# Performance work log

Hardware: AMD Instinct MI355X
Metric: run time of the kernel (lower is better)

## Reference

```python
import jax, jax.numpy as jnp
import numpy as np
import math

D_MODEL = 512
N_HEADS = 8
D_FF = 2048
TOP_FACTOR = 5
LN_EPS = 1e-5


def _layernorm(x, g, b):
    m = jnp.mean(x, axis=-1, keepdims=True)
    v = jnp.mean((x - m) ** 2, axis=-1, keepdims=True)
    return (x - m) / jnp.sqrt(v + LN_EPS) * g + b


def _prob_sparse_attn(q_in, k_in, v_in, wq, bq, wk, bk, wv, bv, wo, bo):
    # weights stored (in, out): y = x @ w + b  (equivalent to torch Linear)
    B, Lq, dm = q_in.shape
    Lk = k_in.shape[1]
    H, D = N_HEADS, dm // N_HEADS
    q = (q_in @ wq + bq).reshape(B, Lq, H, D).transpose(0, 2, 1, 3)  # (B,H,Lq,D)
    k = (k_in @ wk + bk).reshape(B, Lk, H, D).transpose(0, 2, 1, 3)
    v = (v_in @ wv + bv).reshape(B, Lk, H, D).transpose(0, 2, 1, 3)

    qn = q / jnp.linalg.norm(q, axis=-1, keepdims=True)
    kn = k / jnp.linalg.norm(k, axis=-1, keepdims=True)
    # full cosine-similarity matrix, reduced to a row mean (as in the original)
    scores_all = jnp.einsum('bhqd,bhkd->bhqk', qn, kn)
    mean_scores = scores_all.mean(axis=-1)  # (B,H,Lq)

    u = max(1, Lq // TOP_FACTOR)
    _, top_idx = jax.lax.top_k(mean_scores, u)  # (B,H,u)

    q_sel = jnp.take_along_axis(q, top_idx[..., None], axis=2)  # (B,H,u,D)
    scores = jnp.einsum('bhud,bhkd->bhuk', q_sel, k) / math.sqrt(D)
    attn = jax.nn.softmax(scores, axis=-1)
    ctx_sel = jnp.einsum('bhuk,bhkd->bhud', attn, v)  # (B,H,u,D)

    b_ix = jnp.arange(B)[:, None, None]
    h_ix = jnp.arange(H)[None, :, None]
    context = jnp.zeros((B, H, Lq, D), dtype=q.dtype).at[b_ix, h_ix, top_idx].set(ctx_sel)
    out = context.transpose(0, 2, 1, 3).reshape(B, Lq, dm)
    return out @ wo + bo


def _decoder_layer(x, enc_out, p):
    xn = _layernorm(x, p['ln1_g'], p['ln1_b'])
    x = x + _prob_sparse_attn(xn, xn, xn, p['sa_wq'], p['sa_bq'], p['sa_wk'], p['sa_bk'],
                              p['sa_wv'], p['sa_bv'], p['sa_wo'], p['sa_bo'])
    xn = _layernorm(x, p['ln2_g'], p['ln2_b'])
    x = x + _prob_sparse_attn(xn, enc_out, enc_out, p['ca_wq'], p['ca_bq'], p['ca_wk'], p['ca_bk'],
                              p['ca_wv'], p['ca_bv'], p['ca_wo'], p['ca_bo'])
    xn = _layernorm(x, p['ln3_g'], p['ln3_b'])
    h = jax.nn.relu(xn @ p['ff_w1'] + p['ff_b1'])
    return x + (h @ p['ff_w2'] + p['ff_b2'])


def setup_inputs() -> dict:
    key = jax.random.key(0)
    ks = iter(jax.random.split(key, 32))
    B, L = 2, 2048
    dm, dff = D_MODEL, D_FF
    s = 1.0 / math.sqrt(dm)
    inp = {
        'x': jax.random.normal(next(ks), (B, L, dm), jnp.float32),
        'enc_out': jax.random.normal(next(ks), (B, L, dm), jnp.float32),
    }
    for pre in ('sa', 'ca'):
        for nm in ('wq', 'wk', 'wv', 'wo'):
            inp[f'{pre}_{nm}'] = jax.random.normal(next(ks), (dm, dm), jnp.float32) * s
            inp[f'{pre}_{nm[1:] and "b" + nm[1:]}'] = jnp.zeros((dm,), jnp.float32)
    inp['ff_w1'] = jax.random.normal(next(ks), (dm, dff), jnp.float32) * s
    inp['ff_b1'] = jnp.zeros((dff,), jnp.float32)
    inp['ff_w2'] = jax.random.normal(next(ks), (dff, dm), jnp.float32) / math.sqrt(dff)
    inp['ff_b2'] = jnp.zeros((dm,), jnp.float32)
    for i in (1, 2, 3):
        inp[f'ln{i}_g'] = jnp.ones((dm,), jnp.float32)
        inp[f'ln{i}_b'] = jnp.zeros((dm,), jnp.float32)
    return inp


def reference(x, enc_out,
              sa_wq, sa_bq, sa_wk, sa_bk, sa_wv, sa_bv, sa_wo, sa_bo,
              ca_wq, ca_bq, ca_wk, ca_bk, ca_wv, ca_bv, ca_wo, ca_bo,
              ff_w1, ff_b1, ff_w2, ff_b2,
              ln1_g, ln1_b, ln2_g, ln2_b, ln3_g, ln3_b):
    p = dict(sa_wq=sa_wq, sa_bq=sa_bq, sa_wk=sa_wk, sa_bk=sa_bk, sa_wv=sa_wv, sa_bv=sa_bv,
             sa_wo=sa_wo, sa_bo=sa_bo, ca_wq=ca_wq, ca_bq=ca_bq, ca_wk=ca_wk, ca_bk=ca_bk,
             ca_wv=ca_wv, ca_bv=ca_bv, ca_wo=ca_wo, ca_bo=ca_bo,
             ff_w1=ff_w1, ff_b1=ff_b1, ff_w2=ff_w2, ff_b2=ff_b2,
             ln1_g=ln1_g, ln1_b=ln1_b, ln2_g=ln2_g, ln2_b=ln2_b, ln3_g=ln3_g, ln3_b=ln3_b)
    return _decoder_layer(x, enc_out, p)
```

## Files before the change

### kernel.cpp

```cpp
#include <hip/hip_runtime.h>

#define BB 2
#define LL 2048
#define DM 512
#define NH 8
#define DH 64
#define DFF 2048
#define UU 409
#define ROWS (BB*LL)
#define X_ELEMS 2097152
#define NCHUNK 16

typedef unsigned short u16;
typedef __attribute__((ext_vector_type(8))) short short8;
typedef __attribute__((ext_vector_type(4))) float floatx4;

#define G_TOTAL 38200000
__device__ float g_buf[G_TOTAL];
__device__ int   g_isbf16;

#define A_Q     10495488
#define A_K     12592640
#define A_V     14689792
#define A_MKN   25175552
#define A_MS    25176576
#define A_SEL   25209344
#define A_PARTK 25242112
#define A_LIST  25274880
#define A_PO    25281536
#define A_PML   33670144
#define A_CTXF  16786944
#define XN_H    16796672
#define XN_L    18893824
#define CTX_H   33573888
#define CTX_L   35671040
#define ENC_H   37768192
#define ENC_L   39865344
#define AH_H    41962496
#define WT_SAQKV 67864576
#define WT_SAO   69437440
#define WT_CAQ   69961728
#define WT_CAK   70486016
#define WT_CAV   71010304
#define WT_CAO   71534592
#define WT_W1    72058880
#define WT_W2    74156032

__constant__ int c_end[28] = {
    2097152, 4194304, 4456448, 4456960, 4719104, 4719616, 4981760, 4982272,
    5244416, 5244928, 5507072, 5507584, 5769728, 5770240, 6032384, 6032896,
    6295040, 6295552, 7344128, 7346176, 8394752, 8395264, 8395776, 8396288,
    8396800, 8397312, 8397824, 8398336
};
__constant__ int sm_idx[16] = {3,5,7,9,11,13,15,17,19,21,22,23,24,25,26,27};
__constant__ int sm_cum[16] = {64,128,192,256,320,384,448,512,768,832,896,960,1024,1088,1152,1216};
#define XG 262144
#define EG 262144
#define SG 1216

__device__ __forceinline__ float bf2f(u16 x) {
    union { unsigned int u; float f; } c; c.u = ((unsigned int)x) << 16; return c.f;
}
__device__ __forceinline__ u16 f2bf(float f) {
    union { float f; unsigned int u; } c; c.f = f;
    unsigned int u = c.u;
    return (u16)((u + 0x7FFFu + ((u >> 16) & 1u)) >> 16);
}

struct P28 { const void* p[28]; };
struct I3 { int v[3]; };

__global__ void cvt_all(P28 ps) {
    const int f = (((const u16*)ps.p[22])[0] == 0x3F80u) ? 1 : 0;
    if (blockIdx.x == 0 && threadIdx.x == 0) g_isbf16 = f;
    u16* gb16 = (u16*)g_buf;
    int stride = gridDim.x * blockDim.x;
    for (int g = blockIdx.x * blockDim.x + threadIdx.x; g < XG + EG + SG; g += stride) {
        if (g < XG) {
            int e = g * 8;
            if (f) {
                uint4 raw = ((const uint4*)ps.p[0])[g];
                const u16* rr = (const u16*)&raw;
                float v[8] __attribute__((aligned(16)));
#pragma unroll
                for (int i = 0; i < 8; i++) v[i] = bf2f(rr[i]);
                *(float4*)(g_buf + e) = ((const float4*)v)[0];
                *(float4*)(g_buf + e + 4) = ((const float4*)v)[1];
            } else {
                *(uint4*)(g_buf + e)     = ((const uint4*)ps.p[0])[g * 2];
                *(uint4*)(g_buf + e + 4) = ((const uint4*)ps.p[0])[g * 2 + 1];
            }
        } else if (g < XG + EG) {
            int gl = g - XG;
            int e = gl * 8;
            float v[8] __attribute__((aligned(16)));
            if (f) {
                uint4 raw = ((const uint4*)ps.p[1])[gl];
                const u16* rr = (const u16*)&raw;
#pragma unroll
                for (int i = 0; i < 8; i++) v[i] = bf2f(rr[i]);
            } else {
                *(float4*)(v)     = ((const float4*)ps.p[1])[gl * 2];
                *(float4*)(v + 4) = ((const float4*)ps.p[1])[gl * 2 + 1];
            }
            u16 hh[8] __attribute__((aligned(16)));
            u16 lo[8] __attribute__((aligned(16)));
#pragma unroll
            for (int i = 0; i < 8; i++) { u16 hi = f2bf(v[i]); hh[i] = hi; lo[i] = f2bf(v[i] - bf2f(hi)); }
            *(uint4*)(&gb16[ENC_H + e]) = *(const uint4*)hh;
            *(uint4*)(&gb16[ENC_L + e]) = *(const uint4*)lo;
        } else {
            int t = g - XG - EG;
            int si = 0;
            while (t >= sm_cum[si]) si++;
            int s = sm_idx[si];
            int gl = t - (si ? sm_cum[si - 1] : 0);
            int e = gl * 8;
            float* dst = g_buf + c_end[s - 1] + e;
            if (f) {
                uint4 raw = *(const uint4*)((const u16*)ps.p[s] + e);
                const u16* rr = (const u16*)&raw;
#pragma unroll
                for (int i = 0; i < 8; i++) dst[i] = bf2f(rr[i]);
            } else {
                *(uint4*)(dst)     = *(const uint4*)((const float*)ps.p[s] + e);
                *(uint4*)(dst + 4) = *(const uint4*)((const float*)ps.p[s] + e + 4);
            }
        }
    }
}

__constant__ int tj[10][6] = {
    {2,  WT_SAQKV, 0,    512,  786432, 8},
    {4,  WT_SAQKV, 512,  512,  786432, 8},
    {6,  WT_SAQKV, 1024, 512,  786432, 8},
    {8,  WT_SAO,   0,    512,  262144, 8},
    {10, WT_CAQ,   0,    512,  262144, 8},
    {12, WT_CAK,   0,    512,  262144, 8},
    {14, WT_CAV,   0,    512,  262144, 8},
    {16, WT_CAO,   0,    512,  262144, 8},
    {18, WT_W1,    0,    512, 1048576, 32},
    {20, WT_W2,    0,   2048, 1048576, 8},
};
__constant__ int tcum[10] = {64, 128, 192, 256, 320, 384, 448, 512, 768, 1024};
__global__ void transpose_all(P28 ps) {
    const int f = (((const u16*)ps.p[22])[0] == 0x3F80u) ? 1 : 0;
    int bid = blockIdx.x;
    int j = 0;
    while (bid >= tcum[j]) j++;
    int t = bid - (j ? tcum[j - 1] : 0);
    int widx = tj[j][0], wt = tj[j][1], col0 = tj[j][2];
    int K = tj[j][3], lo = tj[j][4], txn = tj[j][5];
    int Nsrc = txn * 64;
    int n0 = (t % txn) * 64, k0 = (t / txn) * 64;
    __shared__ float tb[64][65];
    int c = threadIdx.x & 63, r0 = threadIdx.x >> 6;
    const void* W = ps.p[widx];
    u16* WTh = ((u16*)g_buf) + wt;
    for (int i = 0; i < 16; i++) {
        int r = r0 + 4 * i;
        size_t src = (size_t)(k0 + r) * Nsrc + n0 + c;
        tb[r][c] = f ? bf2f(((const u16*)W)[src]) : ((const float*)W)[src];
    }
    __syncthreads();
    for (int i = 0; i < 16; i++) {
        int r = r0 + 4 * i;
        float v = tb[c][r];
        u16 hi = f2bf(v);
        size_t o = (size_t)(col0 + n0 + r) * K + k0 + c;
        WTh[o] = hi;
        WTh[lo + o] = f2bf(v - bf2f(hi));
    }
}

__global__ void lnorm_k(int x_off, int g_off, int b_off, int yh_u16, int yl_u16) {
    int row = blockIdx.x;
    int tid = threadIdx.x;
    const float* x = g_buf + x_off + (size_t)row * DM;
    float a = x[tid], c = x[tid + 256];
    float s1 = a + c, s2 = a * a + c * c;
    for (int o = 32; o > 0; o >>= 1) { s1 += __shfl_xor(s1, o); s2 += __shfl_xor(s2, o); }
    __shared__ float r1[4], r2[4];
    int wave = tid >> 6, lane = tid & 63;
    if (lane == 0) { r1[wave] = s1; r2[wave] = s2; }
    __syncthreads();
    s1 = r1[0] + r1[1] + r1[2] + r1[3];
    s2 = r2[0] + r2[1] + r2[2] + r2[3];
    float mean = s1 * (1.0f / DM);
    float var  = s2 * (1.0f / DM) - mean * mean;
    float rstd = rsqrtf(var + 1e-5f);
    const float* gg = g_buf + g_off;
    const float* bb = g_buf + b_off;
    u16* yh = ((u16*)g_buf) + yh_u16 + (size_t)row * DM;
    u16* yl = ((u16*)g_buf) + yl_u16 + (size_t)row * DM;
    float v1 = (a - mean) * rstd * gg[tid]       + bb[tid];
    float v2 = (c - mean) * rstd * gg[tid + 256] + bb[tid + 256];
    u16 h1 = f2bf(v1), h2 = f2bf(v2);
    yh[tid] = h1;       yl[tid] = f2bf(v1 - bf2f(h1));
    yh[tid + 256] = h2; yl[tid + 256] = f2bf(v2 - bf2f(h2));
}

template<int WM, bool SPLIT, bool ALZ, bool SEC, bool RELU, bool RESID, bool FINAL, bool OUTH>
__global__ void mgemm_k(int a_u16, int wt_u16_off, I3 boffs, int resid_off,
                        int out_off, void* __restrict__ dext, int M, int N, int K) {
    constexpr int BT_M = WM * 32;
    constexpr int A4 = BT_M * 4;
    __shared__ u16 Ash[BT_M * 40];
    __shared__ u16 Asl[SPLIT ? BT_M * 40 : 8];
    __shared__ u16 Bsh[128 * 40];
    __shared__ u16 Bsl[SPLIT ? 128 * 40 : 8];
    const u16* Ah = ((const u16*)g_buf) + a_u16;
    const u16* Al = Ah + (size_t)M * K;
    const u16* WTh = ((const u16*)g_buf) + wt_u16_off;
    const u16* WTl = WTh + (size_t)N * K;
    const int isbf = g_isbf16;
    const bool use_bl = SPLIT && !isbf;
    const bool use_al = SPLIT && !(ALZ && isbf);
    int tid = threadIdx.x;
    int lane = tid & 63, wid = tid >> 6;
    int wm = wid >> 1, wn = wid & 1;
    int quad = lane >> 4, l15 = lane & 15;
    int m0 = blockIdx.y * BT_M, n0 = blockIdx.x * 128;
    floatx4 acc[WM][4];
#pragma unroll
    for (int i = 0; i < WM; i++)
#pragma unroll
        for (int j = 0; j < 4; j++) acc[i][j] = (floatx4){0.f, 0.f, 0.f, 0.f};
    for (int k0 = 0; k0 < K; k0 += 32) {
#pragma unroll
        for (int i = 0; i < (A4 + 255) / 256; i++) {
            int idx8 = tid + 256 * i;
            if (A4 % 256 == 0 || idx8 < A4) {
                int r = idx8 >> 2, c8 = (idx8 & 3) * 8;
                *(uint4*)(&Ash[r * 40 + c8]) = *(const uint4*)(Ah + (size_t)(m0 + r) * K + k0 + c8);
                if (SPLIT && use_al)
                    *(uint4*)(&Asl[r * 40 + c8]) = *(const uint4*)(Al + (size_t)(m0 + r) * K + k0 + c8);
            }
        }
#pragma unroll
        for (int i = 0; i < 2; i++) {
            int idx8 = tid + 256 * i;
            int r = idx8 >> 2, c8 = (idx8 & 3) * 8;
            *(uint4*)(&Bsh[r * 40 + c8]) = *(const uint4*)(WTh + (size_t)(n0 + r) * K + k0 + c8);
            if (SPLIT && use_bl)
                *(uint4*)(&Bsl[r * 40 + c8]) = *(const uint4*)(WTl + (size_t)(n0 + r) * K + k0 + c8);
        }
        __syncthreads();
        short8 ah[WM], bh[4], al[WM], bl[4];
#pragma unroll
        for (int i = 0; i < WM; i++) {
            int ro = (wm * WM * 16 + i * 16 + l15) * 40 + quad * 8;
            ah[i] = *(const short8*)(&Ash[ro]);
            if (SPLIT && use_al) al[i] = *(const short8*)(&Asl[ro]);
        }
#pragma unroll
        for (int j = 0; j < 4; j++) {
            int ro = (wn * 64 + j * 16 + l15) * 40 + quad * 8;
            bh[j] = *(const short8*)(&Bsh[ro]);
            if (SPLIT && use_bl) bl[j] = *(const short8*)(&Bsl[ro]);
        }
#pragma unroll
        for (int i = 0; i < WM; i++)
#pragma unroll
            for (int j = 0; j < 4; j++) {
                acc[i][j] = __builtin_amdgcn_mfma_f32_16x16x32_bf16(ah[i], bh[j], acc[i][j], 0, 0, 0);
                if constexpr (SPLIT) {
                    if (use_bl)
                        acc[i][j] = __builtin_amdgcn_mfma_f32_16x16x32_bf16(ah[i], bl[j], acc[i][j], 0, 0, 0);
                    if (use_al)
                        acc[i][j] = __builtin_amdgcn_mfma_f32_16x16x32_bf16(al[i], bh[j], acc[i][j], 0, 0, 0);
                }
            }
        __syncthreads();
    }
#pragma unroll
    for (int i = 0; i < WM; i++)
#pragma unroll
        for (int j = 0; j < 4; j++)
#pragma unroll
            for (int r = 0; r < 4; r++) {
                int row = m0 + wm * WM * 16 + i * 16 + quad * 4 + r;
                int col = n0 + wn * 64 + j * 16 + l15;
                int sec = SEC ? (col >> 9) : 0;
                int ci  = SEC ? (col & 511) : col;
                float v = acc[i][j][r] + g_buf[boffs.v[sec] + ci];
                if (RELU) v = fmaxf(v, 0.f);
                if (RESID) v += g_buf[resid_off + (size_t)row * N + col];
                if (FINAL) {
                    if (isbf) ((u16*)dext)[(size_t)row * N + col] = f2bf(v);
                    else      ((float*)dext)[(size_t)row * N + col] = v;
                } else if (OUTH) {
                    ((u16*)g_buf)[out_off + (size_t)row * N + col] = f2bf(v);
                } else if (SEC) {
                    g_buf[out_off + ((size_t)sec * ROWS + row) * 512 + ci] = v;
                } else {
                    g_buf[out_off + (size_t)row * N + col] = v;
                }
            }
}

__global__ void meankn_p1(int k_off, int part_off) {
    int bh = blockIdx.x >> 5, chunk = blockIdx.x & 31;
    int b = bh >> 3, h = bh & 7;
    int wave = threadIdx.x >> 6, lane = threadIdx.x & 63;
    const float* base = g_buf + k_off + (size_t)b * LL * DM + (size_t)h * DH + lane;
    float acc = 0.f;
    for (int t = 0; t < 16; t++) {
        int j = chunk * 64 + wave * 16 + t;
        float kv = base[(size_t)j * DM];
        float s = kv * kv;
        for (int o = 32; o > 0; o >>= 1) s += __shfl_xor(s, o);
        acc += kv / sqrtf(fmaxf(s, 1e-30f));
    }
    __shared__ float red[4][64];
    red[wave][lane] = acc;
    __syncthreads();
    if (threadIdx.x < 64)
        g_buf[part_off + (size_t)blockIdx.x * 64 + threadIdx.x] =
            red[0][threadIdx.x] + red[1][threadIdx.x] + red[2][threadIdx.x] + red[3][threadIdx.x];
}
__global__ void meankn_p2(int part_off, int mkn_off) {
    int bh = blockIdx.x; int lane = threadIdx.x;
    float s = 0.f;
    for (int c = 0; c < 32; c++) s += g_buf[part_off + (size_t)(bh * 32 + c) * 64 + lane];
    g_buf[mkn_off + bh * 64 + lane] = s * (1.0f / LL);
}

__global__ void mscore_k(int q_off, int mkn_off, int ms_off) {
    int row = blockIdx.x * 4 + (threadIdx.x >> 6);
    int lane = threadIdx.x & 63;
    int q = row & (LL - 1);
    int bh = row >> 11;
    int b = bh >> 3, h = bh & 7;
    float qv = g_buf[q_off + ((size_t)b * LL + q) * DM + h * DH + lane];
    float m = g_buf[mkn_off + bh * 64 + lane];
    float s = qv * qv, d = qv * m;
    for (int o = 32; o > 0; o >>= 1) { s += __shfl_xor(s, o); d += __shfl_xor(d, o); }
    if (lane == 0) g_buf[ms_off + row] = d / sqrtf(fmaxf(s, 1e-30f));
}

__global__ void topsel_k(int ms_off, int sel_off, int u) {
    __shared__ float s[LL];
    int bh = blockIdx.y, chunk = blockIdx.x;
    for (int i = threadIdx.x; i < LL; i += 256) s[i] = g_buf[ms_off + bh * LL + i];
    __syncthreads();
    int il = threadIdx.x >> 2;
    int i = chunk * 64 + il;
    int jq = threadIdx.x & 3;
    float si = s[i];
    int cnt = 0;
    for (int t = 0; t < 512; t++) {
        int j = jq * 512 + t;
        float sj = s[j];
        cnt += (sj > si) || (sj == si && j < i);
    }
    cnt += __shfl_xor(cnt, 1);
    cnt += __shfl_xor(cnt, 2);
    if (jq == 0) ((int*)(g_buf + sel_off))[bh * LL + i] = (cnt < u) ? 1 : 0;
}

__global__ void compact_k(int sel_off, int list_off) {
    __shared__ int cnts[256];
    __shared__ int pref[256];
    int bh = blockIdx.x, tid = threadIdx.x;
    const int* sel = (const int*)(g_buf + sel_off) + bh * LL;
    int* list = (int*)(g_buf + list_off) + bh * 416;
    int c = 0;
    for (int j = 0; j < 8; j++) c += sel[tid * 8 + j];
    cnts[tid] = c;
    __syncthreads();
    if (tid == 0) { int run = 0; for (int i = 0; i < 256; i++) { pref[i] = run; run += cnts[i]; } }
    __syncthreads();
    int base = pref[tid];
    for (int j = 0; j < 8; j++) {
        int i = tid * 8 + j;
        if (sel[i]) list[base++] = i;
    }
}

__global__ void zero_k(int off, int n) {
    int i = blockIdx.x * blockDim.x + threadIdx.x;
    int st = gridDim.x * blockDim.x;
    for (; i < n; i += st) g_buf[off + i] = 0.f;
}

__global__ __launch_bounds__(256, 2) void attn_flash(int q_off, int k_off, int v_off,
        int list_off, int po_off, int pml_off, int u) {
    int bh = blockIdx.y, b = bh >> 3, h = bh & 7;
    int chunk = blockIdx.z;
    int tid = threadIdx.x, lane = tid & 63, w = tid >> 6;
    int quad = lane >> 4, l15 = lane & 15;
    const int* list = (const int*)(g_buf + list_off);

    short8 qh[4][2], ql[4][2];
#pragma unroll
    for (int g = 0; g < 4; g++) {
        int slot_q = blockIdx.x * 256 + w * 64 + g * 16 + l15;
        int qidx = list[bh * 416 + (slot_q < u ? slot_q : u - 1)];
        const float* qp = g_buf + q_off + ((size_t)b * LL + qidx) * DM + h * DH;
#pragma unroll
        for (int d2 = 0; d2 < 2; d2++) {
            float v[8] __attribute__((aligned(16)));
            *(float4*)(v)     = *(const float4*)(qp + d2 * 32 + quad * 8);
            *(float4*)(v + 4) = *(const float4*)(qp + d2 * 32 + quad * 8 + 4);
            u16 hh[8] __attribute__((aligned(16)));
            u16 lo[8] __attribute__((aligned(16)));
#pragma unroll
            for (int j = 0; j < 8; j++) {
                float s = v[j] * 0.125f;
                u16 hi = f2bf(s); hh[j] = hi; lo[j] = f2bf(s - bf2f(hi));
            }
            qh[g][d2] = *(const short8*)hh; ql[g][d2] = *(const short8*)lo;
        }
    }

    __shared__ u16 Ksh[64 * 68], Ksl[64 * 68];
    __shared__ u16 Vth[64 * 68], Vtl[64 * 68];
    __shared__ float smbuf[4352];

    float m_run[4][4], l_run[4][4];
    floatx4 acc_o[4][4];
#pragma unroll
    for (int g = 0; g < 4; g++)
#pragma unroll
        for (int r = 0; r < 4; r++) {
            m_run[g][r] = -3.0e38f; l_run[g][r] = 0.f;
            acc_o[g][r] = (floatx4){0.f, 0.f, 0.f, 0.f};
        }

    for (int kt = 0; kt < 2; kt++) {
        int row0 = chunk * 128 + kt * 64;
        __syncthreads();
        {
            int tok = tid >> 2, c = (tid & 3) * 16;
            const float* kp = g_buf + k_off + ((size_t)(b * LL + row0 + tok)) * DM + h * DH + c;
            float v[16] __attribute__((aligned(16)));
#pragma unroll
            for (int i = 0; i < 4; i++) *(float4*)(v + 4 * i) = *(const float4*)(kp + 4 * i);
            u16 hh[16] __attribute__((aligned(16)));
            u16 lo[16] __attribute__((aligned(16)));
#pragma unroll
            for (int i = 0; i < 16; i++) { u16 hi = f2bf(v[i]); hh[i] = hi; lo[i] = f2bf(v[i] - bf2f(hi)); }
            *(uint4*)(&Ksh[tok * 68 + c])     = ((const uint4*)hh)[0];
            *(uint4*)(&Ksh[tok * 68 + c + 8]) = ((const uint4*)hh)[1];
            *(uint4*)(&Ksl[tok * 68 + c])     = ((const uint4*)lo)[0];
            *(uint4*)(&Ksl[tok * 68 + c + 8]) = ((const uint4*)lo)[1];
            const float* vp = g_buf + v_off + ((size_t)(b * LL + row0 + tok)) * DM + h * DH + c;
#pragma unroll
            for (int i = 0; i < 4; i++)
                *(float4*)(&smbuf[tok * 68 + c + 4 * i]) = *(const float4*)(vp + 4 * i);
        }
        __syncthreads();
        {
            int d = tid >> 2, ck = (tid & 3) * 16;
            u16 hh[16] __attribute__((aligned(16)));
            u16 lo[16] __attribute__((aligned(16)));
#pragma unroll
            for (int i = 0; i < 16; i++) {
                float x = smbuf[(ck + i) * 68 + d];
                u16 hi = f2bf(x); hh[i] = hi; lo[i] = f2bf(x - bf2f(hi));
            }
            *(uint4*)(&Vth[d * 68 + ck])     = ((const uint4*)hh)[0];
            *(uint4*)(&Vth[d * 68 + ck + 8]) = ((const uint4*)hh)[1];
            *(uint4*)(&Vtl[d * 68 + ck])     = ((const uint4*)lo)[0];
            *(uint4*)(&Vtl[d * 68 + ck + 8]) = ((const uint4*)lo)[1];
        }
        __syncthreads();
        float* ps = smbuf + w * 1088;
#pragma unroll
        for (int g = 0; g < 4; g++) {
            floatx4 sacc[4];
#pragma unroll
            for (int t = 0; t < 4; t++) {
                sacc[t] = (floatx4){0.f, 0.f, 0.f, 0.f};
#pragma unroll
                for (int d2 = 0; d2 < 2; d2++) {
                    int ro = (t * 16 + l15) * 68 + d2 * 32 + quad * 8;
                    short8 kh = *(const short8*)(&Ksh[ro]);
                    short8 kl = *(const short8*)(&Ksl[ro]);
                    sacc[t] = __builtin_amdgcn_mfma_f32_16x16x32_bf16(qh[g][d2], kh, sacc[t], 0, 0, 0);
                    sacc[t] = __builtin_amdgcn_mfma_f32_16x16x32_bf16(qh[g][d2], kl, sacc[t], 0, 0, 0);
                    sacc[t] = __builtin_amdgcn_mfma_f32_16x16x32_bf16(ql[g][d2], kh, sacc[t], 0, 0, 0);
                }
            }
            float alpha[4];
#pragma unroll
            for (int r = 0; r < 4; r++) {
                float mx = fmaxf(fmaxf(sacc[0][r], sacc[1][r]), fmaxf(sacc[2][r], sacc[3][r]));
                for (int o = 1; o < 16; o <<= 1) mx = fmaxf(mx, __shfl_xor(mx, o));
                float mn = fmaxf(m_run[g][r], mx);
                alpha[r] = __expf(m_run[g][r] - mn);
                m_run[g][r] = mn;
                float ls = 0.f;
#pragma unroll
                for (int t = 0; t < 4; t++) {
                    float p = __expf(sacc[t][r] - mn);
                    sacc[t][r] = p;
                    ls += p;
                }
                for (int o = 1; o < 16; o <<= 1) ls += __shfl_xor(ls, o);
                l_run[g][r] = l_run[g][r] * alpha[r] + ls;
            }
#pragma unroll
            for (int t = 0; t < 4; t++)
#pragma unroll
                for (int r = 0; r < 4; r++)
                    ps[(quad * 4 + r) * 68 + t * 16 + l15] = sacc[t][r];
#pragma unroll
            for (int j = 0; j < 4; j++)
#pragma unroll
                for (int r = 0; r < 4; r++) acc_o[g][j][r] *= alpha[r];
#pragma unroll
            for (int s2 = 0; s2 < 2; s2++) {
                float pv[8] __attribute__((aligned(16)));
                *(float4*)(pv)     = *(const float4*)(&ps[l15 * 68 + s2 * 32 + quad * 8]);
                *(float4*)(pv + 4) = *(const float4*)(&ps[l15 * 68 + s2 * 32 + quad * 8 + 4]);
                u16 ph[8] __attribute__((aligned(16)));
                u16 pl[8] __attribute__((aligned(16)));
#pragma unroll
                for (int j = 0; j < 8; j++) { u16 hi = f2bf(pv[j]); ph[j] = hi; pl[j] = f2bf(pv[j] - bf2f(hi)); }
                short8 phv = *(const short8*)ph, plv = *(const short8*)pl;
#pragma unroll
                for (int j = 0; j < 4; j++) {
                    int ro = (j * 16 + l15) * 68 + s2 * 32 + quad * 8;
                    short8 vh = *(const short8*)(&Vth[ro]);
                    short8 vl = *(const short8*)(&Vtl[ro]);
                    acc_o[g][j] = __builtin_amdgcn_mfma_f32_16x16x32_bf16(phv, vh, acc_o[g][j], 0, 0, 0);
                    acc_o[g][j] = __builtin_amdgcn_mfma_f32_16x16x32_bf16(phv, vl, acc_o[g][j], 0, 0, 0);
                    acc_o[g][j] = __builtin_amdgcn_mfma_f32_16x16x32_bf16(plv, vh, acc_o[g][j], 0, 0, 0);
                }
            }
        }
    }
#pragma unroll
    for (int g = 0; g < 4; g++)
#pragma unroll
        for (int r = 0; r < 4; r++) {
            int slot = blockIdx.x * 256 + w * 64 + g * 16 + quad * 4 + r;
            if (slot >= u) continue;
            size_t rec = ((size_t)(bh * 16 + chunk)) * 512 + slot;
            float* po = g_buf + po_off + rec * 64;
#pragma unroll
            for (int j = 0; j < 4; j++) po[j * 16 + l15] = acc_o[g][j][r];
            if (l15 == 0) {
                float* pml = g_buf + pml_off + rec * 2;
                pml[0] = m_run[g][r]; pml[1] = l_run[g][r];
            }
        }
}

__global__ void attn_combine(int po_off, int pml_off, int list_off, int u) {
    int bh = blockIdx.y;
    int b = bh >> 3, h = bh & 7;
    int tid = threadIdx.x;
    int qi = tid >> 4;
    int kb = tid & 15;
    int ds = kb * 4;
    int slot = blockIdx.x * 16 + qi;
    if (slot >= u) return;
    int qidx = ((const int*)(g_buf + list_off))[bh * 416 + slot];
    float m = -3.0e38f;
#pragma unroll
    for (int c = 0; c < NCHUNK; c++)
        m = fmaxf(m, g_buf[pml_off + (((size_t)(bh * 16 + c)) * 512 + slot) * 2]);
    float l = 0.f, O0 = 0.f, O1 = 0.f, O2 = 0.f, O3 = 0.f;
#pragma unroll
    for (int c = 0; c < NCHUNK; c++) {
        size_t rec = ((size_t)(bh * 16 + c)) * 512 + slot;
        const float* pml = g_buf + pml_off + rec * 2;
        float a = __expf(pml[0] - m);
        l += a * pml[1];
        float4 o = *(const float4*)(g_buf + po_off + rec * 64 + ds);
        O0 += a * o.x; O1 += a * o.y; O2 += a * o.z; O3 += a * o.w;
    }
    float inv = 1.0f / l;
    float o0 = O0 * inv, o1 = O1 * inv, o2 = O2 * inv, o3 = O3 * inv;
    size_t idx = ((size_t)b * LL + qidx) * DM + h * DH + ds;
    ushort4 hv, lv;
    hv.x = f2bf(o0); lv.x = f2bf(o0 - bf2f(hv.x));
    hv.y = f2bf(o1); lv.y = f2bf(o1 - bf2f(hv.y));
    hv.z = f2bf(o2); lv.z = f2bf(o2 - bf2f(hv.z));
    hv.w = f2bf(o3); lv.w = f2bf(o3 - bf2f(hv.w));
    *(ushort4*)(((u16*)g_buf) + CTX_H + idx) = hv;
    *(ushort4*)(((u16*)g_buf) + CTX_L + idx) = lv;
}

extern "C" void kernel_launch(void* const* d_in, const int* in_sizes, int n_in,
                              void* d_out, int out_size, void* d_ws, size_t ws_size,
                              hipStream_t stream) {
    static const int SZ[28] = {
        2097152, 2097152,
        262144, 512, 262144, 512, 262144, 512, 262144, 512,
        262144, 512, 262144, 512, 262144, 512, 262144, 512,
        1048576, 2048, 1048576, 512,
        512, 512, 512, 512, 512, 512
    };
    int OFF[28];
    int cur = 0;
    for (int i = 0; i < 28; i++) { OFF[i] = cur; cur += SZ[i]; }

    P28 ps;
    for (int i = 0; i < 28; i++) ps.p[i] = d_in[i];
    cvt_all<<<2048, 256, 0, stream>>>(ps);
    transpose_all<<<1024, 256, 0, stream>>>(ps);

    auto select_attend = [&](void) {
        meankn_p1<<<16 * 32, 256, 0, stream>>>(A_K, A_PARTK);
        meankn_p2<<<16, 64, 0, stream>>>(A_PARTK, A_MKN);
        mscore_k<<<(BB * NH * LL) / 4, 256, 0, stream>>>(A_Q, A_MKN, A_MS);
        topsel_k<<<dim3(32, 16), 256, 0, stream>>>(A_MS, A_SEL, UU);
        compact_k<<<BB * NH, 256, 0, stream>>>(A_SEL, A_LIST);
        zero_k<<<1024, 256, 0, stream>>>(A_CTXF, X_ELEMS);
        attn_flash<<<dim3(2, 16, NCHUNK), 256, 0, stream>>>(A_Q, A_K, A_V, A_LIST, A_PO, A_PML, UU);
        attn_combine<<<dim3(26, 16), 256, 0, stream>>>(A_PO, A_PML, A_LIST, UU);
    };

    lnorm_k<<<ROWS, 256, 0, stream>>>(OFF[0], OFF[22], OFF[23], XN_H, XN_L);
    mgemm_k<2, true, false, true, false, false, false, false><<<dim3(12, 64), 256, 0, stream>>>(
        XN_H, WT_SAQKV, I3{{OFF[3], OFF[5], OFF[7]}}, 0, A_Q, nullptr, ROWS, 1536, 512);
    select_attend();
    mgemm_k<1, true, false, false, false, true, false, false><<<dim3(4, 128), 256, 0, stream>>>(
        CTX_H, WT_SAO, I3{{OFF[9], 0, 0}}, OFF[0], OFF[0], nullptr, ROWS, 512, 512);

    lnorm_k<<<ROWS, 256, 0, stream>>>(OFF[0], OFF[24], OFF[25], XN_H, XN_L);
    mgemm_k<1, true, false, false, false, false, false, false><<<dim3(4, 128), 256, 0, stream>>>(
        XN_H, WT_CAQ, I3{{OFF[11], 0, 0}}, 0, A_Q, nullptr, ROWS, 512, 512);
    mgemm_k<1, true, true, false, false, false, false, false><<<dim3(4, 128), 256, 0, stream>>>(
        ENC_H, WT_CAK, I3{{OFF[13], 0, 0}}, 0, A_K, nullptr, ROWS, 512, 512);
    mgemm_k<1, false, false, false, false, false, false, false><<<dim3(4, 128), 256, 0, stream>>>(
        ENC_H, WT_CAV, I3{{OFF[15], 0, 0}}, 0, A_V, nullptr, ROWS, 512, 512);
    select_attend();
    mgemm_k<1, false, false, false, false, true, false, false><<<dim3(4, 128), 256, 0, stream>>>(
        CTX_H, WT_CAO, I3{{OFF[17], 0, 0}}, OFF[0], OFF[0], nullptr, ROWS, 512, 512);

    lnorm_k<<<ROWS, 256, 0, stream>>>(OFF[0], OFF[26], OFF[27], XN_H, XN_L);
    mgemm_k<4, false, false, false, true, false, false, true><<<dim3(16, 32), 256, 0, stream>>>(
        XN_H, WT_W1, I3{{OFF[19], 0, 0}}, 0, AH_H, nullptr, ROWS, 2048, 512);
    mgemm_k<1, false, false, false, false, true, true, false><<<dim3(4, 128), 256, 0, stream>>>(
        AH_H, WT_W2, I3{{OFF[21], 0, 0}}, OFF[0], 0, d_out, ROWS, 512, 2048);
}
```

Before: 585.3 us.

## Fuse prep kernels, merge cross-attn K/V GEMM, and cut sparse-attention launches

Merges the input conversion and weight transpose into one prep kernel, and fuses the cross-attention K and V projections into a single sectioned GEMM. It folds mean-key reduction into the score kernel and has top-k selection write the compact list and rank directly, dropping the compact and zero kernels. The combine step zero-fills unselected rows itself. Attention blocks are made smaller (more blocks), and cross-attention drops the third bf16 split product. The aim is fewer launches and less redundant work, at the cost of some precision in cross-attention and more indexing logic.

```diff
diff --git a/kernel.cpp b/kernel.cpp
--- a/kernel.cpp
+++ b/kernel.cpp
@@ -24,7 +24,7 @@
 #define A_V     14689792
 #define A_MKN   25175552
 #define A_MS    25176576
-#define A_SEL   25209344
+#define A_RANK  25209344
 #define A_PARTK 25242112
 #define A_LIST  25274880
 #define A_PO    25281536
@@ -40,8 +40,7 @@
 #define WT_SAQKV 67864576
 #define WT_SAO   69437440
 #define WT_CAQ   69961728
-#define WT_CAK   70486016
-#define WT_CAV   71010304
+#define WT_CAKV  70486016
 #define WT_CAO   71534592
 #define WT_W1    72058880
 #define WT_W2    74156032
@@ -70,12 +69,54 @@
 struct P28 { const void* p[28]; };
 struct I3 { int v[3]; };
 
-__global__ void cvt_all(P28 ps) {
+__constant__ int tj[10][6] = {
+    {2,  WT_SAQKV, 0,    512,  786432, 8},
+    {4,  WT_SAQKV, 512,  512,  786432, 8},
+    {6,  WT_SAQKV, 1024, 512,  786432, 8},
+    {8,  WT_SAO,   0,    512,  262144, 8},
+    {10, WT_CAQ,   0,    512,  262144, 8},
+    {12, WT_CAKV,  0,    512,  524288, 8},
+    {14, WT_CAKV,  512,  512,  524288, 8},
+    {16, WT_CAO,   0,    512,  262144, 8},
+    {18, WT_W1,    0,    512, 1048576, 32},
+    {20, WT_W2,    0,   2048, 1048576, 8},
+};
+__constant__ int tcum[10] = {64, 128, 192, 256, 320, 384, 448, 512, 768, 1024};
+__global__ void prep_all(P28 ps) {
     const int f = (((const u16*)ps.p[22])[0] == 0x3F80u) ? 1 : 0;
     if (blockIdx.x == 0 && threadIdx.x == 0) g_isbf16 = f;
     u16* gb16 = (u16*)g_buf;
-    int stride = gridDim.x * blockDim.x;
-    for (int g = blockIdx.x * blockDim.x + threadIdx.x; g < XG + EG + SG; g += stride) {
+    if (blockIdx.x < 1024) {
+        int bid = blockIdx.x;
+        int j = 0;
+        while (bid >= tcum[j]) j++;
+        int t = bid - (j ? tcum[j - 1] : 0);
+        int widx = tj[j][0], wt = tj[j][1], col0 = tj[j][2];
+        int K = tj[j][3], lo = tj[j][4], txn = tj[j][5];
+        int Nsrc = txn * 64;
+        int n0 = (t % txn) * 64, k0 = (t / txn) * 64;
+        __shared__ float tb[64][65];
+        int c = threadIdx.x & 63, r0 = threadIdx.x >> 6;
+        const void* W = ps.p[widx];
+        u16* WTh = gb16 + wt;
+        for (int i = 0; i < 16; i++) {
+            int r = r0 + 4 * i;
+            size_t src = (size_t)(k0 + r) * Nsrc + n0 + c;
+            tb[r][c] = f ? bf2f(((const u16*)W)[src]) : ((const float*)W)[src];
+        }
+        __syncthreads();
+        for (int i = 0; i < 16; i++) {
+            int r = r0 + 4 * i;
+            float v = tb[c][r];
+            u16 hi = f2bf(v);
+            size_t o = (size_t)(col0 + n0 + r) * K + k0 + c;
+            WTh[o] = hi;
+            WTh[lo + o] = f2bf(v - bf2f(hi));
+        }
+        return;
+    }
+    int stride = 2048 * blockDim.x;
+    for (int g = (blockIdx.x - 1024) * blockDim.x + threadIdx.x; g < XG + EG + SG; g += stride) {
         if (g < XG) {
             int e = g * 8;
             if (f) {
@@ -127,49 +168,6 @@
                 *(uint4*)(dst + 4) = *(const uint4*)((const float*)ps.p[s] + e + 4);
             }
         }
-    }
-}
-
-__constant__ int tj[10][6] = {
-    {2,  WT_SAQKV, 0,    512,  786432, 8},
-    {4,  WT_SAQKV, 512,  512,  786432, 8},
-    {6,  WT_SAQKV, 1024, 512,  786432, 8},
-    {8,  WT_SAO,   0,    512,  262144, 8},
-    {10, WT_CAQ,   0,    512,  262144, 8},
-    {12, WT_CAK,   0,    512,  262144, 8},
-    {14, WT_CAV,   0,    512,  262144, 8},
-    {16, WT_CAO,   0,    512,  262144, 8},
-    {18, WT_W1,    0,    512, 1048576, 32},
-    {20, WT_W2,    0,   2048, 1048576, 8},
-};
-__constant__ int tcum[10] = {64, 128, 192, 256, 320, 384, 448, 512, 768, 1024};
-__global__ void transpose_all(P28 ps) {
-    const int f = (((const u16*)ps.p[22])[0] == 0x3F80u) ? 1 : 0;
-    int bid = blockIdx.x;
-    int j = 0;
-    while (bid >= tcum[j]) j++;
-    int t = bid - (j ? tcum[j - 1] : 0);
-    int widx = tj[j][0], wt = tj[j][1], col0 = tj[j][2];
-    int K = tj[j][3], lo = tj[j][4], txn = tj[j][5];
-    int Nsrc = txn * 64;
-    int n0 = (t % txn) * 64, k0 = (t / txn) * 64;
-    __shared__ float tb[64][65];
-    int c = threadIdx.x & 63, r0 = threadIdx.x >> 6;
-    const void* W = ps.p[widx];
-    u16* WTh = ((u16*)g_buf) + wt;
-    for (int i = 0; i < 16; i++) {
-        int r = r0 + 4 * i;
-        size_t src = (size_t)(k0 + r) * Nsrc + n0 + c;
-        tb[r][c] = f ? bf2f(((const u16*)W)[src]) : ((const float*)W)[src];
-    }
-    __syncthreads();
-    for (int i = 0; i < 16; i++) {
-        int r = r0 + 4 * i;
-        float v = tb[c][r];
-        u16 hi = f2bf(v);
-        size_t o = (size_t)(col0 + n0 + r) * K + k0 + c;
-        WTh[o] = hi;
-        WTh[lo + o] = f2bf(v - bf2f(hi));
     }
 }
 
@@ -200,8 +198,8 @@
     yh[tid + 256] = h2; yl[tid + 256] = f2bf(v2 - bf2f(h2));
 }
 
-template<int WM, bool SPLIT, bool ALZ, bool SEC, bool RELU, bool RESID, bool FINAL, bool OUTH>
-__global__ void mgemm_k(int a_u16, int wt_u16_off, I3 boffs, int resid_off,
+template<int WM, bool SPLIT, bool SEC, bool RELU, bool RESID, bool FINAL, bool OUTH>
+__global__ void mgemm_k(I3 a_offs, I3 splt, I3 alz, int wt_u16_off, I3 boffs, int resid_off,
                         int out_off, void* __restrict__ dext, int M, int N, int K) {
     constexpr int BT_M = WM * 32;
     constexpr int A4 = BT_M * 4;
@@ -209,13 +207,14 @@
     __shared__ u16 Asl[SPLIT ? BT_M * 40 : 8];
     __shared__ u16 Bsh[128 * 40];
     __shared__ u16 Bsl[SPLIT ? 128 * 40 : 8];
-    const u16* Ah = ((const u16*)g_buf) + a_u16;
+    int sec_blk = SEC ? ((blockIdx.x * 128) >> 9) : 0;
+    const u16* Ah = ((const u16*)g_buf) + a_offs.v[sec_blk];
     const u16* Al = Ah + (size_t)M * K;
     const u16* WTh = ((const u16*)g_buf) + wt_u16_off;
     const u16* WTl = WTh + (size_t)N * K;
     const int isbf = g_isbf16;
-    const bool use_bl = SPLIT && !isbf;
-    const bool use_al = SPLIT && !(ALZ && isbf);
+    const bool use_al = SPLIT && splt.v[sec_blk] && !(alz.v[sec_blk] && isbf);
+    const bool use_bl = SPLIT && splt.v[sec_blk] && !isbf;
     int tid = threadIdx.x;
     int lane = tid & 63, wid = tid >> 6;
     int wm = wid >> 1, wn = wid & 1;
@@ -287,8 +286,8 @@
                 if (RELU) v = fmaxf(v, 0.f);
                 if (RESID) v += g_buf[resid_off + (size_t)row * N + col];
                 if (FINAL) {
-                    if (isbf) ((u16*)dext)[(size_t)row * N + col] = f2bf(v);
-                    else      ((float*)dext)[(size_t)row * N + col] = v;
+                    if (g_isbf16) ((u16*)dext)[(size_t)row * N + col] = f2bf(v);
+                    else          ((float*)dext)[(size_t)row * N + col] = v;
                 } else if (OUTH) {
                     ((u16*)g_buf)[out_off + (size_t)row * N + col] = f2bf(v);
                 } else if (SEC) {
@@ -319,27 +318,30 @@
         g_buf[part_off + (size_t)blockIdx.x * 64 + threadIdx.x] =
             red[0][threadIdx.x] + red[1][threadIdx.x] + red[2][threadIdx.x] + red[3][threadIdx.x];
 }
-__global__ void meankn_p2(int part_off, int mkn_off) {
-    int bh = blockIdx.x; int lane = threadIdx.x;
-    float s = 0.f;
-    for (int c = 0; c < 32; c++) s += g_buf[part_off + (size_t)(bh * 32 + c) * 64 + lane];
-    g_buf[mkn_off + bh * 64 + lane] = s * (1.0f / LL);
-}
-
-__global__ void mscore_k(int q_off, int mkn_off, int ms_off) {
-    int row = blockIdx.x * 4 + (threadIdx.x >> 6);
-    int lane = threadIdx.x & 63;
-    int q = row & (LL - 1);
-    int bh = row >> 11;
-    int b = bh >> 3, h = bh & 7;
-    float qv = g_buf[q_off + ((size_t)b * LL + q) * DM + h * DH + lane];
-    float m = g_buf[mkn_off + bh * 64 + lane];
-    float s = qv * qv, d = qv * m;
-    for (int o = 32; o > 0; o >>= 1) { s += __shfl_xor(s, o); d += __shfl_xor(d, o); }
-    if (lane == 0) g_buf[ms_off + row] = d / sqrtf(fmaxf(s, 1e-30f));
-}
-
-__global__ void topsel_k(int ms_off, int sel_off, int u) {
+
+__global__ void mscore_k(int q_off, int part_off, int ms_off) {
+    int bh = blockIdx.y, b = bh >> 3, h = bh & 7;
+    int tid = threadIdx.x;
+    __shared__ float mk[64];
+    if (tid < 64) {
+        float s = 0.f;
+        for (int c = 0; c < 32; c++) s += g_buf[part_off + (size_t)(bh * 32 + c) * 64 + tid];
+        mk[tid] = s * (1.0f / LL);
+    }
+    __syncthreads();
+    int w = tid >> 6, lane = tid & 63;
+    float m = mk[lane];
+#pragma unroll
+    for (int it = 0; it < 8; it++) {
+        int row = blockIdx.x * 32 + it * 4 + w;
+        float qv = g_buf[q_off + ((size_t)b * LL + row) * DM + h * DH + lane];
+        float s = qv * qv, d = qv * m;
+        for (int o = 32; o > 0; o >>= 1) { s += __shfl_xor(s, o); d += __shfl_xor(d, o); }
+        if (lane == 0) g_buf[ms_off + bh * LL + row] = d / sqrtf(fmaxf(s, 1e-30f));
+    }
+}
+
+__global__ void topsel_k(int ms_off, int list_off, int rank_off, int u) {
     __shared__ float s[LL];
     int bh = blockIdx.y, chunk = blockIdx.x;
     for (int i = threadIdx.x; i < LL; i += 256) s[i] = g_buf[ms_off + bh * LL + i];
@@ -356,35 +358,16 @@
     }
     cnt += __shfl_xor(cnt, 1);
     cnt += __shfl_xor(cnt, 2);
-    if (jq == 0) ((int*)(g_buf + sel_off))[bh * LL + i] = (cnt < u) ? 1 : 0;
-}
-
-__global__ void compact_k(int sel_off, int list_off) {
-    __shared__ int cnts[256];
-    __shared__ int pref[256];
-    int bh = blockIdx.x, tid = threadIdx.x;
-    const int* sel = (const int*)(g_buf + sel_off) + bh * LL;
-    int* list = (int*)(g_buf + list_off) + bh * 416;
-    int c = 0;
-    for (int j = 0; j < 8; j++) c += sel[tid * 8 + j];
-    cnts[tid] = c;
-    __syncthreads();
-    if (tid == 0) { int run = 0; for (int i = 0; i < 256; i++) { pref[i] = run; run += cnts[i]; } }
-    __syncthreads();
-    int base = pref[tid];
-    for (int j = 0; j < 8; j++) {
-        int i = tid * 8 + j;
-        if (sel[i]) list[base++] = i;
-    }
-}
-
-__global__ void zero_k(int off, int n) {
-    int i = blockIdx.x * blockDim.x + threadIdx.x;
-    int st = gridDim.x * blockDim.x;
-    for (; i < n; i += st) g_buf[off + i] = 0.f;
-}
-
-__global__ __launch_bounds__(256, 2) void attn_flash(int q_off, int k_off, int v_off,
+    if (jq == 0) {
+        int* list = (int*)(g_buf + list_off);
+        int* rank = (int*)(g_buf + rank_off);
+        if (cnt < u) { list[bh * 416 + cnt] = i; rank[bh * LL + i] = cnt; }
+        else rank[bh * LL + i] = -1;
+    }
+}
+
+template<bool S3>
+__global__ __launch_bounds__(256) void attn_flash(int q_off, int k_off, int v_off,
         int list_off, int po_off, int pml_off, int u) {
     int bh = blockIdx.y, b = bh >> 3, h = bh & 7;
     int chunk = blockIdx.z;
@@ -392,10 +375,10 @@
     int quad = lane >> 4, l15 = lane & 15;
     const int* list = (const int*)(g_buf + list_off);
 
-    short8 qh[4][2], ql[4][2];
-#pragma unroll
-    for (int g = 0; g < 4; g++) {
-        int slot_q = blockIdx.x * 256 + w * 64 + g * 16 + l15;
+    short8 qh[2][2], ql[2][2];
+#pragma unroll
+    for (int g = 0; g < 2; g++) {
+        int slot_q = blockIdx.x * 128 + w * 32 + g * 16 + l15;
         int qidx = list[bh * 416 + (slot_q < u ? slot_q : u - 1)];
         const float* qp = g_buf + q_off + ((size_t)b * LL + qidx) * DM + h * DH;
 #pragma unroll
@@ -414,14 +397,16 @@
         }
     }
 
-    __shared__ u16 Ksh[64 * 68], Ksl[64 * 68];
-    __shared__ u16 Vth[64 * 68], Vtl[64 * 68];
+    __shared__ u16 Ksh[64 * 68];
+    __shared__ u16 Ksl[S3 ? 64 * 68 : 8];
+    __shared__ u16 Vth[64 * 68];
+    __shared__ u16 Vtl[S3 ? 64 * 68 : 8];
     __shared__ float smbuf[4352];
 
-    float m_run[4][4], l_run[4][4];
-    floatx4 acc_o[4][4];
-#pragma unroll
-    for (int g = 0; g < 4; g++)
+    float m_run[2][4], l_run[2][4];
+    floatx4 acc_o[2][4];
+#pragma unroll
+    for (int g = 0; g < 2; g++)
 #pragma unroll
         for (int r = 0; r < 4; r++) {
             m_run[g][r] = -3.0e38f; l_run[g][r] = 0.f;
@@ -438,13 +423,17 @@
 #pragma unroll
             for (int i = 0; i < 4; i++) *(float4*)(v + 4 * i) = *(const float4*)(kp + 4 * i);
             u16 hh[16] __attribute__((aligned(16)));
-            u16 lo[16] __attribute__((aligned(16)));
-#pragma unroll
-            for (int i = 0; i < 16; i++) { u16 hi = f2bf(v[i]); hh[i] = hi; lo[i] = f2bf(v[i] - bf2f(hi)); }
+#pragma unroll
+            for (int i = 0; i < 16; i++) hh[i] = f2bf(v[i]);
             *(uint4*)(&Ksh[tok * 68 + c])     = ((const uint4*)hh)[0];
             *(uint4*)(&Ksh[tok * 68 + c + 8]) = ((const uint4*)hh)[1];
-            *(uint4*)(&Ksl[tok * 68 + c])     = ((const uint4*)lo)[0];
-            *(uint4*)(&Ksl[tok * 68 + c + 8]) = ((const uint4*)lo)[1];
+            if constexpr (S3) {
+                u16 lo[16] __attribute__((aligned(16)));
+#pragma unroll
+                for (int i = 0; i < 16; i++) lo[i] = f2bf(v[i] - bf2f(hh[i]));
+                *(uint4*)(&Ksl[tok * 68 + c])     = ((const uint4*)lo)[0];
+                *(uint4*)(&Ksl[tok * 68 + c + 8]) = ((const uint4*)lo)[1];
+            }
             const float* vp = g_buf + v_off + ((size_t)(b * LL + row0 + tok)) * DM + h * DH + c;
 #pragma unroll
             for (int i = 0; i < 4; i++)
@@ -454,21 +443,23 @@
         {
             int d = tid >> 2, ck = (tid & 3) * 16;
             u16 hh[16] __attribute__((aligned(16)));
-            u16 lo[16] __attribute__((aligned(16)));
-#pragma unroll
-            for (int i = 0; i < 16; i++) {
-                float x = smbuf[(ck + i) * 68 + d];
-                u16 hi = f2bf(x); hh[i] = hi; lo[i] = f2bf(x - bf2f(hi));
-            }
+            float xv[16];
+#pragma unroll
+            for (int i = 0; i < 16; i++) { xv[i] = smbuf[(ck + i) * 68 + d]; hh[i] = f2bf(xv[i]); }
             *(uint4*)(&Vth[d * 68 + ck])     = ((const uint4*)hh)[0];
             *(uint4*)(&Vth[d * 68 + ck + 8]) = ((const uint4*)hh)[1];
-            *(uint4*)(&Vtl[d * 68 + ck])     = ((const uint4*)lo)[0];
-            *(uint4*)(&Vtl[d * 68 + ck + 8]) = ((const uint4*)lo)[1];
+            if constexpr (S3) {
+                u16 lo[16] __attribute__((aligned(16)));
+#pragma unroll
+                for (int i = 0; i < 16; i++) lo[i] = f2bf(xv[i] - bf2f(hh[i]));
+                *(uint4*)(&Vtl[d * 68 + ck])     = ((const uint4*)lo)[0];
+                *(uint4*)(&Vtl[d * 68 + ck + 8]) = ((const uint4*)lo)[1];
+            }
         }
         __syncthreads();
         float* ps = smbuf + w * 1088;
 #pragma unroll
-        for (int g = 0; g < 4; g++) {
+        for (int g = 0; g < 2; g++) {
             floatx4 sacc[4];
 #pragma unroll
             for (int t = 0; t < 4; t++) {
@@ -477,10 +468,12 @@
                 for (int d2 = 0; d2 < 2; d2++) {
                     int ro = (t * 16 + l15) * 68 + d2 * 32 + quad * 8;
                     short8 kh = *(const short8*)(&Ksh[ro]);
-                    short8 kl = *(const short8*)(&Ksl[ro]);
                     sacc[t] = __builtin_amdgcn_mfma_f32_16x16x32_bf16(qh[g][d2], kh, sacc[t], 0, 0, 0);
-                    sacc[t] = __builtin_amdgcn_mfma_f32_16x16x32_bf16(qh[g][d2], kl, sacc[t], 0, 0, 0);
                     sacc[t] = __builtin_amdgcn_mfma_f32_16x16x32_bf16(ql[g][d2], kh, sacc[t], 0, 0, 0);
+                    if constexpr (S3) {
+                        short8 kl = *(const short8*)(&Ksl[ro]);
+                        sacc[t] = __builtin_amdgcn_mfma_f32_16x16x32_bf16(qh[g][d2], kl, sacc[t], 0, 0, 0);
+                    }
                 }
             }
             float alpha[4];
@@ -524,19 +517,21 @@
                 for (int j = 0; j < 4; j++) {
                     int ro = (j * 16 + l15) * 68 + s2 * 32 + quad * 8;
                     short8 vh = *(const short8*)(&Vth[ro]);
-                    short8 vl = *(const short8*)(&Vtl[ro]);
                     acc_o[g][j] = __builtin_amdgcn_mfma_f32_16x16x32_bf16(phv, vh, acc_o[g][j], 0, 0, 0);
-                    acc_o[g][j] = __builtin_amdgcn_mfma_f32_16x16x32_bf16(phv, vl, acc_o[g][j], 0, 0, 0);
                     acc_o[g][j] = __builtin_amdgcn_mfma_f32_16x16x32_bf16(plv, vh, acc_o[g][j], 0, 0, 0);
+                    if constexpr (S3) {
+                        short8 vl = *(const short8*)(&Vtl[ro]);
+                        acc_o[g][j] = __builtin_amdgcn_mfma_f32_16x16x32_bf16(phv, vl, acc_o[g][j], 0, 0, 0);
+                    }
                 }
             }
         }
     }
 #pragma unroll
-    for (int g = 0; g < 4; g++)
+    for (int g = 0; g < 2; g++)
 #pragma unroll
         for (int r = 0; r < 4; r++) {
-            int slot = blockIdx.x * 256 + w * 64 + g * 16 + quad * 4 + r;
+            int slot = blockIdx.x * 128 + w * 32 + g * 16 + quad * 4 + r;
             if (slot >= u) continue;
             size_t rec = ((size_t)(bh * 16 + chunk)) * 512 + slot;
             float* po = g_buf + po_off + rec * 64;
@@ -549,24 +544,30 @@
         }
 }
 
-__global__ void attn_combine(int po_off, int pml_off, int list_off, int u) {
+__global__ void attn_combine(int po_off, int pml_off, int rank_off, int u) {
     int bh = blockIdx.y;
     int b = bh >> 3, h = bh & 7;
     int tid = threadIdx.x;
     int qi = tid >> 4;
     int kb = tid & 15;
     int ds = kb * 4;
-    int slot = blockIdx.x * 16 + qi;
-    if (slot >= u) return;
-    int qidx = ((const int*)(g_buf + list_off))[bh * 416 + slot];
+    int row = blockIdx.x * 16 + qi;
+    int rank = ((const int*)(g_buf + rank_off))[bh * LL + row];
+    size_t idx = ((size_t)b * LL + row) * DM + h * DH + ds;
+    if (rank < 0) {
+        ushort4 z = {0, 0, 0, 0};
+        *(ushort4*)(((u16*)g_buf) + CTX_H + idx) = z;
+        *(ushort4*)(((u16*)g_buf) + CTX_L + idx) = z;
+        return;
+    }
     float m = -3.0e38f;
 #pragma unroll
     for (int c = 0; c < NCHUNK; c++)
-        m = fmaxf(m, g_buf[pml_off + (((size_t)(bh * 16 + c)) * 512 + slot) * 2]);
+        m = fmaxf(m, g_buf[pml_off + (((size_t)(bh * 16 + c)) * 512 + rank) * 2]);
     float l = 0.f, O0 = 0.f, O1 = 0.f, O2 = 0.f, O3 = 0.f;
 #pragma unroll
     for (int c = 0; c < NCHUNK; c++) {
-        size_t rec = ((size_t)(bh * 16 + c)) * 512 + slot;
+        size_t rec = ((size_t)(bh * 16 + c)) * 512 + rank;
         const float* pml = g_buf + pml_off + rec * 2;
         float a = __expf(pml[0] - m);
         l += a * pml[1];
@@ -575,7 +576,6 @@
     }
     float inv = 1.0f / l;
     float o0 = O0 * inv, o1 = O1 * inv, o2 = O2 * inv, o3 = O3 * inv;
-    size_t idx = ((size_t)b * LL + qidx) * DM + h * DH + ds;
     ushort4 hv, lv;
     hv.x = f2bf(o0); lv.x = f2bf(o0 - bf2f(hv.x));
     hv.y = f2bf(o1); lv.y = f2bf(o1 - bf2f(hv.y));
@@ -601,41 +601,45 @@
 
     P28 ps;
     for (int i = 0; i < 28; i++) ps.p[i] = d_in[i];
-    cvt_all<<<2048, 256, 0, stream>>>(ps);
-    transpose_all<<<1024, 256, 0, stream>>>(ps);
-
-    auto select_attend = [&](void) {
+    prep_all<<<3072, 256, 0, stream>>>(ps);
+
+    auto select_attend = [&](bool sa) {
         meankn_p1<<<16 * 32, 256, 0, stream>>>(A_K, A_PARTK);
-        meankn_p2<<<16, 64, 0, stream>>>(A_PARTK, A_MKN);
-        mscore_k<<<(BB * NH * LL) / 4, 256, 0, stream>>>(A_Q, A_MKN, A_MS);
-        topsel_k<<<dim3(32, 16), 256, 0, stream>>>(A_MS, A_SEL, UU);
-        compact_k<<<BB * NH, 256, 0, stream>>>(A_SEL, A_LIST);
-        zero_k<<<1024, 256, 0, stream>>>(A_CTXF, X_ELEMS);
-        attn_flash<<<dim3(2, 16, NCHUNK), 256, 0, stream>>>(A_Q, A_K, A_V, A_LIST, A_PO, A_PML, UU);
-        attn_combine<<<dim3(26, 16), 256, 0, stream>>>(A_PO, A_PML, A_LIST, UU);
+        mscore_k<<<dim3(64, 16), 256, 0, stream>>>(A_Q, A_PARTK, A_MS);
+        topsel_k<<<dim3(32, 16), 256, 0, stream>>>(A_MS, A_LIST, A_RANK, UU);
+        if (sa)
+            attn_flash<true><<<dim3(4, 16, NCHUNK), 256, 0, stream>>>(A_Q, A_K, A_V, A_LIST, A_PO, A_PML, UU);
+        else
+            attn_flash<false><<<dim3(4, 16, NCHUNK), 256, 0, stream>>>(A_Q, A_K, A_V, A_LIST, A_PO, A_PML, UU);
+        attn_combine<<<dim3(128, 16), 256, 0, stream>>>(A_PO, A_PML, A_RANK, UU);
     };
 
     lnorm_k<<<ROWS, 256, 0, stream>>>(OFF[0], OFF[22], OFF[23], XN_H, XN_L);
-    mgemm_k<2, true, false, true, false, false, false, false><<<dim3(12, 64), 256, 0, stream>>>(
-        XN_H, WT_SAQKV, I3{{OFF[3], OFF[5], OFF[7]}}, 0, A_Q, nullptr, ROWS, 1536, 512);
-    select_attend();
-    mgemm_k<1, true, false, false, false, true, false, false><<<dim3(4, 128), 256, 0, stream>>>(
-        CTX_H, WT_SAO, I3{{OFF[9], 0, 0}}, OFF[0], OFF[0], nullptr, ROWS, 512, 512);
+    mgemm_k<2, true, true, false, false, false, false><<<dim3(12, 64), 256, 0, stream>>>(
+        I3{{XN_H, XN_H, XN_H}}, I3{{1, 1, 1}}, I3{{0, 0, 0}},
+        WT_SAQKV, I3{{OFF[3], OFF[5], OFF[7]}}, 0, A_Q, nullptr, ROWS, 1536, 512);
+    select_attend(true);
+    mgemm_k<1, true, false, false, true, false, false><<<dim3(4, 128), 256, 0, stream>>>(
+        I3{{CTX_H, 0, 0}}, I3{{1, 0, 0}}, I3{{0, 0, 0}},
+        WT_SAO, I3{{OFF[9], 0, 0}}, OFF[0], OFF[0], nullptr, ROWS, 512, 512);
 
     lnorm_k<<<ROWS, 256, 0, stream>>>(OFF[0], OFF[24], OFF[25], XN_H, XN_L);
-    mgemm_k<1, true, false, false, false, false, false, false><<<dim3(4, 128), 256, 0, stream>>>(
-        XN_H, WT_CAQ, I3{{OFF[11], 0, 0}}, 0, A_Q, nullptr, ROWS, 512, 512);
-    mgemm_k<1, true, true, false, false, false, false, false><<<dim3(4, 128), 256, 0, stream>>>(
-        ENC_H, WT_CAK, I3{{OFF[13], 0, 0}}, 0, A_K, nullptr, ROWS, 512, 512);
-    mgemm_k<1, false, false, false, false, false, false, false><<<dim3(4, 128), 256, 0, stream>>>(
-        ENC_H, WT_CAV, I3{{OFF[15], 0, 0}}, 0, A_V, nullptr, ROWS, 512, 512);
-    select_attend();
-    mgemm_k<1, false, false, false, false, true, false, false><<<dim3(4, 128), 256, 0, stream>>>(
-        CTX_H, WT_CAO, I3{{OFF[17], 0, 0}}, OFF[0], OFF[0], nullptr, ROWS, 512, 512);
+    mgemm_k<1, true, false, false, false, false, false><<<dim3(4, 128), 256, 0, stream>>>(
+        I3{{XN_H, 0, 0}}, I3{{1, 0, 0}}, I3{{0, 0, 0}},
+        WT_CAQ, I3{{OFF[11], 0, 0}}, 0, A_Q, nullptr, ROWS, 512, 512);
+    mgemm_k<2, true, true, false, false, false, false><<<dim3(8, 64), 256, 0, stream>>>(
+        I3{{ENC_H, ENC_H, ENC_H}}, I3{{1, 0, 0}}, I3{{1, 0, 0}},
+        WT_CAKV, I3{{OFF[13], OFF[15], 0}}, 0, A_K, nullptr, ROWS, 1024, 512);
+    select_attend(false);
+    mgemm_k<1, false, false, false, true, false, false><<<dim3(4, 128), 256, 0, stream>>>(
+        I3{{CTX_H, 0, 0}}, I3{{0, 0, 0}}, I3{{0, 0, 0}},
+        WT_CAO, I3{{OFF[17], 0, 0}}, OFF[0], OFF[0], nullptr, ROWS, 512, 512);
 
     lnorm_k<<<ROWS, 256, 0, stream>>>(OFF[0], OFF[26], OFF[27], XN_H, XN_L);
-    mgemm_k<4, false, false, false, true, false, false, true><<<dim3(16, 32), 256, 0, stream>>>(
-        XN_H, WT_W1, I3{{OFF[19], 0, 0}}, 0, AH_H, nullptr, ROWS, 2048, 512);
-    mgemm_k<1, false, false, false, false, true, true, false><<<dim3(4, 128), 256, 0, stream>>>(
-        AH_H, WT_W2, I3{{OFF[21], 0, 0}}, OFF[0], 0, d_out, ROWS, 512, 2048);
-}
+    mgemm_k<4, false, false, true, false, false, true><<<dim3(16, 32), 256, 0, stream>>>(
+        I3{{XN_H, 0, 0}}, I3{{0, 0, 0}}, I3{{0, 0, 0}},
+        WT_W1, I3{{OFF[19], 0, 0}}, 0, AH_H, nullptr, ROWS, 2048, 512);
+    mgemm_k<1, false, false, false, true, true, false><<<dim3(4, 128), 256, 0, stream>>>(
+        I3{{AH_H, 0, 0}}, I3{{0, 0, 0}}, I3{{0, 0, 0}},
+        WT_W2, I3{{OFF[21], 0, 0}}, OFF[0], 0, d_out, ROWS, 512, 2048);
+}
```

Measured after the change: 564.9 us. 1.04x faster.
